# Kernel tuning notes

Hardware: AMD Instinct MI355X
Metric: run time of the kernel (lower is better)

Reference implementation:

```python
import jax, jax.numpy as jnp
import numpy as np

T, B, I, H = 2048, 128, 10, 512  # timesteps, batch, input_size, hidden_size


def setup_inputs() -> dict:
    key = jax.random.key(0)
    ks = jax.random.split(key, 7)
    s = 1.0 / np.sqrt(H)  # torch LSTMCell default init scale
    return {
        "x": jax.random.normal(ks[0], (T, B, I), dtype=jnp.float32),
        "hx": jax.random.normal(ks[1], (B, H), dtype=jnp.float32) * 0.1,
        "cx": jax.random.normal(ks[2], (B, H), dtype=jnp.float32) * 0.1,
        "W_ih": jax.random.uniform(ks[3], (4 * H, I), jnp.float32, -s, s),
        "W_hh": jax.random.uniform(ks[4], (4 * H, H), jnp.float32, -s, s),
        "b_ih": jax.random.uniform(ks[5], (4 * H,), jnp.float32, -s, s),
        "b_hh": jax.random.uniform(ks[6], (4 * H,), jnp.float32, -s, s),
    }


def reference(x, hx, cx, W_ih, W_hh, b_ih, b_hh):
    # Standard LSTMCell recurrence (PyTorch gate order: i, f, g, o).
    bias = b_ih + b_hh  # [4H]

    def step(carry, xt):
        h, c = carry  # [B,H], [B,H]
        gates = xt @ W_ih.T + h @ W_hh.T + bias  # [B,4H]
        i, f, g, o = jnp.split(gates, 4, axis=-1)
        i = jax.nn.sigmoid(i)
        f = jax.nn.sigmoid(f)
        g = jnp.tanh(g)
        o = jax.nn.sigmoid(o)
        c = f * c + i * g
        h = o * jnp.tanh(c)
        return (h, c), None

    (h, c), _ = jax.lax.scan(step, (hx, cx), x)  # scan over T
    # Original returns (x, (hx, cx)) where x == final hx.
    return (h, (h, c))
```

## Files before the change

### kernel.cpp

```cpp
#include <hip/hip_runtime.h>
#include <hip/hip_fp16.h>

#define T_STEPS 2048
#define B_SZ 128
#define I_SZ 10
#define H_SZ 512

#define NGRP 8
#define GWG 8
#define NWG (NGRP * GWG)
#define BSLICE 16
#define WCOL 64
#define NTHR 512

typedef _Float16 f16x8 __attribute__((ext_vector_type(8)));
typedef float f32x4 __attribute__((ext_vector_type(4)));
typedef float f32x2 __attribute__((ext_vector_type(2)));
typedef unsigned u32x4 __attribute__((ext_vector_type(4)));
typedef unsigned u32x2 __attribute__((ext_vector_type(2)));
typedef unsigned long long u64t;

__global__ void clear_hbuf_kernel(u64t* p) {
    const int i = blockIdx.x * 256 + threadIdx.x;
    #pragma unroll
    for (int k = 0; k < 4; ++k)
        __hip_atomic_store(p + i + k * 16384, 0ull,
                           __ATOMIC_RELAXED, __HIP_MEMORY_SCOPE_AGENT);
}

__global__ __launch_bounds__(NTHR, 2) void lstm_persistent(
    const float* __restrict__ x,
    const float* __restrict__ hx,
    const float* __restrict__ cx,
    const float* __restrict__ W_ih,
    const float* __restrict__ W_hh,
    const float* __restrict__ b_ih,
    const float* __restrict__ b_hh,
    float* __restrict__ out,
    u64t* hbuf)
{
    __shared__ _Float16 h_stage[BSLICE][520];
    __shared__ float lds_g[4 * WCOL][17];

    const int wg   = blockIdx.x;
    const int g    = wg >> 3;
    const int wgin = wg & 7;
    const int tid  = threadIdx.x;
    const int wid  = tid >> 6;
    const int lane = tid & 63;
    const int fr_col = lane & 15;
    const int fr_kg  = lane >> 4;

    int gcL[2], wr[2];
    #pragma unroll
    for (int f = 0; f < 2; ++f) {
        gcL[f] = wid * 32 + f * 16 + fr_col;
        wr[f]  = (gcL[f] >> 6) * H_SZ + wgin * WCOL + (gcL[f] & 63);
    }

    f16x8 wf[2][16];
    #pragma unroll
    for (int f = 0; f < 2; ++f)
        #pragma unroll
        for (int c = 0; c < 16; ++c) {
            const float* p = W_hh + (size_t)wr[f] * H_SZ + c * 32 + fr_kg * 8;
            f16x8 w;
            #pragma unroll
            for (int e = 0; e < 8; ++e) w[e] = (_Float16)p[e];
            wf[f][c] = w;
        }

    float wih[2][I_SZ], bias[2];
    #pragma unroll
    for (int f = 0; f < 2; ++f) {
        #pragma unroll
        for (int i = 0; i < I_SZ; ++i) wih[f][i] = W_ih[wr[f] * I_SZ + i];
        bias[f] = b_ih[wr[f]] + b_hh[wr[f]];
    }

    const int orow  = tid >> 5;
    const int ocol  = wgin * WCOL + 2 * (tid & 31);
    const int gbrow = g * BSLICE + orow;
    const size_t my_q = (size_t)orow * 256 + (ocol >> 1);

    float c0 = cx[gbrow * H_SZ + ocol];
    float c1 = cx[gbrow * H_SZ + ocol + 1];
    float h0 = hx[gbrow * H_SZ + ocol];
    float h1 = hx[gbrow * H_SZ + ocol + 1];

    int   st_row[4], st_p[4];
    bool  st_own[4];
    #pragma unroll
    for (int j = 0; j < 4; ++j) {
        const int q = wid * 512 + j * 128 + lane * 2;
        st_row[j] = q >> 8;
        st_p[j]   = q & 255;
        st_own[j] = ((st_p[j] >> 5) == wgin);
    }

    const int sent_idx = 15 * 256 + (lane & 7) * 32 + 31;

    {
        u64t* hb0 = hbuf + (size_t)g * (BSLICE * 256);
        union { _Float16 hp[2]; unsigned u; } pk;
        pk.hp[0] = (_Float16)h0; pk.hp[1] = (_Float16)h1;
        __hip_atomic_store(hb0 + my_q, ((u64t)1u << 32) | pk.u,
                           __ATOMIC_RELAXED, __HIP_MEMORY_SCOPE_AGENT);
        *(unsigned*)&h_stage[orow][ocol] = pk.u;
    }

    #pragma unroll 1
    for (int t = 0; t < T_STEPS; ++t) {
        f32x4 acc[2];
        #pragma unroll
        for (int r = 0; r < 4; ++r) {
            const int grow = g * BSLICE + fr_kg * 4 + r;
            const f32x2* xp = (const f32x2*)(x + ((size_t)t * B_SZ + grow) * I_SZ);
            const f32x2 a0 = xp[0], a1 = xp[1], a2 = xp[2], a3 = xp[3], a4 = xp[4];
            #pragma unroll
            for (int f = 0; f < 2; ++f) {
                float s = bias[f];
                s += a0.x*wih[f][0] + a0.y*wih[f][1] + a1.x*wih[f][2] + a1.y*wih[f][3]
                   + a2.x*wih[f][4] + a2.y*wih[f][5] + a3.x*wih[f][6] + a3.y*wih[f][7]
                   + a4.x*wih[f][8] + a4.y*wih[f][9];
                acc[f][r] = s;
            }
        }

        const u64t* hb = hbuf + ((size_t)(t & 1) * NGRP + g) * (BSLICE * 256);
        const unsigned tgt = (unsigned)(t + 1);

        if (wid == 0) {
            const u64t* sp = hb + sent_idx;
            for (;;) {
                u64t sv = __hip_atomic_load(sp, __ATOMIC_RELAXED,
                                            __HIP_MEMORY_SCOPE_AGENT);
                if (__all((unsigned)(sv >> 32) >= tgt)) break;
                __builtin_amdgcn_s_sleep(1);
            }
        }
        __syncthreads();

        {
            const char* sp = (const char*)hb + wid * 4096 + lane * 16;
            u32x4 q0, q1, q2, q3;
            bool done = false;
            for (;;) {
                if (!done) {
                    asm volatile(
                        "global_load_dwordx4 %0, %4, off sc0 sc1\n\t"
                        "global_load_dwordx4 %1, %4, off offset:1024 sc0 sc1\n\t"
                        "global_load_dwordx4 %2, %4, off offset:2048 sc0 sc1\n\t"
                        "global_load_dwordx4 %3, %4, off offset:3072 sc0 sc1\n\t"
                        "s_waitcnt vmcnt(0)"
                        : "=&v"(q0), "=&v"(q1), "=&v"(q2), "=&v"(q3)
                        : "v"(sp) : "memory");
                    done = (st_own[0] || (q0.y >= tgt && q0.w >= tgt)) &&
                           (st_own[1] || (q1.y >= tgt && q1.w >= tgt)) &&
                           (st_own[2] || (q2.y >= tgt && q2.w >= tgt)) &&
                           (st_own[3] || (q3.y >= tgt && q3.w >= tgt));
                }
                if (__all(done)) break;
                __builtin_amdgcn_s_sleep(1);
            }
            if (!st_own[0]) *(u32x2*)&h_stage[st_row[0]][st_p[0] * 2] = (u32x2){q0.x, q0.z};
            if (!st_own[1]) *(u32x2*)&h_stage[st_row[1]][st_p[1] * 2] = (u32x2){q1.x, q1.z};
            if (!st_own[2]) *(u32x2*)&h_stage[st_row[2]][st_p[2] * 2] = (u32x2){q2.x, q2.z};
            if (!st_own[3]) *(u32x2*)&h_stage[st_row[3]][st_p[3] * 2] = (u32x2){q3.x, q3.z};
        }
        __syncthreads();

        #pragma unroll
        for (int c = 0; c < 16; ++c) {
            const f16x8 a = *(const f16x8*)&h_stage[fr_col][c * 32 + fr_kg * 8];
            acc[0] = __builtin_amdgcn_mfma_f32_16x16x32_f16(a, wf[0][c], acc[0], 0, 0, 0);
            acc[1] = __builtin_amdgcn_mfma_f32_16x16x32_f16(a, wf[1][c], acc[1], 0, 0, 0);
        }

        #pragma unroll
        for (int f = 0; f < 2; ++f)
            #pragma unroll
            for (int r = 0; r < 4; ++r)
                lds_g[gcL[f]][fr_kg * 4 + r] = acc[f][r];
        __syncthreads();

        {
            const int cl = 2 * (tid & 31);
            const float i0 = lds_g[0 * WCOL + cl][orow],     f0 = lds_g[1 * WCOL + cl][orow];
            const float g0 = lds_g[2 * WCOL + cl][orow],     o0 = lds_g[3 * WCOL + cl][orow];
            const float i1 = lds_g[0 * WCOL + cl + 1][orow], f1 = lds_g[1 * WCOL + cl + 1][orow];
            const float g1 = lds_g[2 * WCOL + cl + 1][orow], o1 = lds_g[3 * WCOL + cl + 1][orow];

            const float ig0 = 1.f / (1.f + __expf(-i0));
            const float fg0 = 1.f / (1.f + __expf(-f0));
            const float eg0 = __expf(-2.f * g0);
            const float tg0 = (1.f - eg0) / (1.f + eg0);
            const float og0 = 1.f / (1.f + __expf(-o0));
            const float ig1 = 1.f / (1.f + __expf(-i1));
            const float fg1 = 1.f / (1.f + __expf(-f1));
            const float eg1 = __expf(-2.f * g1);
            const float tg1 = (1.f - eg1) / (1.f + eg1);
            const float og1 = 1.f / (1.f + __expf(-o1));

            c0 = fg0 * c0 + ig0 * tg0;
            c1 = fg1 * c1 + ig1 * tg1;
            const float e0 = __expf(-2.f * c0), e1 = __expf(-2.f * c1);
            h0 = og0 * (1.f - e0) / (1.f + e0);
            h1 = og1 * (1.f - e1) / (1.f + e1);

            if (t < T_STEPS - 1) {
                u64t* hbn = hbuf + ((size_t)((t + 1) & 1) * NGRP + g) * (BSLICE * 256);
                union { _Float16 hp[2]; unsigned u; } pk;
                pk.hp[0] = (_Float16)h0; pk.hp[1] = (_Float16)h1;
                __hip_atomic_store(hbn + my_q,
                                   ((u64t)(unsigned)(t + 2) << 32) | pk.u,
                                   __ATOMIC_RELAXED, __HIP_MEMORY_SCOPE_AGENT);
                *(unsigned*)&h_stage[orow][ocol] = pk.u;
            }
        }
    }

    out[gbrow * H_SZ + ocol]                       = h0;
    out[gbrow * H_SZ + ocol + 1]                   = h1;
    out[B_SZ * H_SZ + gbrow * H_SZ + ocol]         = h0;
    out[B_SZ * H_SZ + gbrow * H_SZ + ocol + 1]     = h1;
    out[2 * B_SZ * H_SZ + gbrow * H_SZ + ocol]     = c0;
    out[2 * B_SZ * H_SZ + gbrow * H_SZ + ocol + 1] = c1;
}

extern "C" void kernel_launch(void* const* d_in, const int* in_sizes, int n_in,
                              void* d_out, int out_size, void* d_ws, size_t ws_size,
                              hipStream_t stream) {
    const float* x    = (const float*)d_in[0];
    const float* hx   = (const float*)d_in[1];
    const float* cx   = (const float*)d_in[2];
    const float* W_ih = (const float*)d_in[3];
    const float* W_hh = (const float*)d_in[4];
    const float* b_ih = (const float*)d_in[5];
    const float* b_hh = (const float*)d_in[6];
    float* out = (float*)d_out;

    u64t* hbuf = (u64t*)d_ws;

    clear_hbuf_kernel<<<64, 256, 0, stream>>>(hbuf);
    lstm_persistent<<<NWG, NTHR, 0, stream>>>(x, hx, cx, W_ih, W_hh, b_ih, b_hh,
                                              out, hbuf);
}
```

Baseline: 6.492 ms.

## Compute all four gates per wave to remove LDS gate exchange and a barrier

Each wave now owns 16 hidden columns across all four gates (i,f,g,o), so its MFMA accumulators hold every gate needed for the cell update. The LDS gate-transpose buffer and one __syncthreads per timestep go away, and the block shrinks to 256 threads with 4x16 f16 weight fragments held in registers. Each wave also stages all of h from global memory, including its own columns, with eight loads per poll instead of four. The cost is higher register pressure per thread and a few lane shuffles to pack h pairs before the tagged stores.

Measured after the change: 7.337 ms. 13.0% more time.

```diff
diff --git a/kernel.cpp b/kernel.cpp
--- a/kernel.cpp
+++ b/kernel.cpp
@@ -11,7 +11,7 @@
 #define NWG (NGRP * GWG)
 #define BSLICE 16
 #define WCOL 64
-#define NTHR 512
+#define NTHR 256
 
 typedef _Float16 f16x8 __attribute__((ext_vector_type(8)));
 typedef float f32x4 __attribute__((ext_vector_type(4)));
@@ -28,7 +28,7 @@
                            __ATOMIC_RELAXED, __HIP_MEMORY_SCOPE_AGENT);
 }
 
-__global__ __launch_bounds__(NTHR, 2) void lstm_persistent(
+__global__ __launch_bounds__(NTHR, 1) void lstm_persistent(
     const float* __restrict__ x,
     const float* __restrict__ hx,
     const float* __restrict__ cx,
@@ -40,7 +40,6 @@
     u64t* hbuf)
 {
     __shared__ _Float16 h_stage[BSLICE][520];
-    __shared__ float lds_g[4 * WCOL][17];
 
     const int wg   = blockIdx.x;
     const int g    = wg >> 3;
@@ -51,79 +50,75 @@
     const int fr_col = lane & 15;
     const int fr_kg  = lane >> 4;
 
-    int gcL[2], wr[2];
-    #pragma unroll
-    for (int f = 0; f < 2; ++f) {
-        gcL[f] = wid * 32 + f * 16 + fr_col;
-        wr[f]  = (gcL[f] >> 6) * H_SZ + wgin * WCOL + (gcL[f] & 63);
-    }
-
-    f16x8 wf[2][16];
-    #pragma unroll
-    for (int f = 0; f < 2; ++f)
+    const int colL = wid * 16 + fr_col;
+    const int gcol = wgin * WCOL + colL;
+
+    f16x8 wf[4][16];
+    #pragma unroll
+    for (int gt = 0; gt < 4; ++gt)
         #pragma unroll
         for (int c = 0; c < 16; ++c) {
-            const float* p = W_hh + (size_t)wr[f] * H_SZ + c * 32 + fr_kg * 8;
+            const float* p = W_hh + (size_t)(gt * H_SZ + gcol) * H_SZ + c * 32 + fr_kg * 8;
             f16x8 w;
             #pragma unroll
             for (int e = 0; e < 8; ++e) w[e] = (_Float16)p[e];
-            wf[f][c] = w;
-        }
-
-    float wih[2][I_SZ], bias[2];
-    #pragma unroll
-    for (int f = 0; f < 2; ++f) {
-        #pragma unroll
-        for (int i = 0; i < I_SZ; ++i) wih[f][i] = W_ih[wr[f] * I_SZ + i];
-        bias[f] = b_ih[wr[f]] + b_hh[wr[f]];
-    }
-
-    const int orow  = tid >> 5;
-    const int ocol  = wgin * WCOL + 2 * (tid & 31);
-    const int gbrow = g * BSLICE + orow;
-    const size_t my_q = (size_t)orow * 256 + (ocol >> 1);
-
-    float c0 = cx[gbrow * H_SZ + ocol];
-    float c1 = cx[gbrow * H_SZ + ocol + 1];
-    float h0 = hx[gbrow * H_SZ + ocol];
-    float h1 = hx[gbrow * H_SZ + ocol + 1];
-
-    int   st_row[4], st_p[4];
-    bool  st_own[4];
-    #pragma unroll
-    for (int j = 0; j < 4; ++j) {
-        const int q = wid * 512 + j * 128 + lane * 2;
-        st_row[j] = q >> 8;
-        st_p[j]   = q & 255;
-        st_own[j] = ((st_p[j] >> 5) == wgin);
-    }
+            wf[gt][c] = w;
+        }
+
+    float wih[4][I_SZ], bias[4];
+    #pragma unroll
+    for (int gt = 0; gt < 4; ++gt) {
+        #pragma unroll
+        for (int i = 0; i < I_SZ; ++i) wih[gt][i] = W_ih[(gt * H_SZ + gcol) * I_SZ + i];
+        bias[gt] = b_ih[gt * H_SZ + gcol] + b_hh[gt * H_SZ + gcol];
+    }
+
+    float cst[4], hst[4];
+    #pragma unroll
+    for (int r = 0; r < 4; ++r) {
+        const int gbrow = g * BSLICE + fr_kg * 4 + r;
+        cst[r] = cx[gbrow * H_SZ + gcol];
+        hst[r] = hx[gbrow * H_SZ + gcol];
+    }
+
+    const int cp = wgin * 32 + wid * 8 + (fr_col >> 1);
+    const bool odd = (fr_col & 1);
+    const int prow0 = fr_kg * 4 + (odd ? 2 : 0);
 
     const int sent_idx = 15 * 256 + (lane & 7) * 32 + 31;
 
     {
         u64t* hb0 = hbuf + (size_t)g * (BSLICE * 256);
-        union { _Float16 hp[2]; unsigned u; } pk;
-        pk.hp[0] = (_Float16)h0; pk.hp[1] = (_Float16)h1;
-        __hip_atomic_store(hb0 + my_q, ((u64t)1u << 32) | pk.u,
-                           __ATOMIC_RELAXED, __HIP_MEMORY_SCOPE_AGENT);
-        *(unsigned*)&h_stage[orow][ocol] = pk.u;
+        #pragma unroll
+        for (int j = 0; j < 2; ++j) {
+            const float give = odd ? hst[j] : hst[2 + j];
+            const float hp   = __shfl_xor(give, 1);
+            const float own  = odd ? hst[2 + j] : hst[j];
+            const float lo = odd ? hp : own;
+            const float hi = odd ? own : hp;
+            union { _Float16 f[2]; unsigned u; } pk;
+            pk.f[0] = (_Float16)lo; pk.f[1] = (_Float16)hi;
+            __hip_atomic_store(hb0 + (size_t)(prow0 + j) * 256 + cp,
+                               ((u64t)1u << 32) | pk.u,
+                               __ATOMIC_RELAXED, __HIP_MEMORY_SCOPE_AGENT);
+        }
     }
 
     #pragma unroll 1
     for (int t = 0; t < T_STEPS; ++t) {
-        f32x4 acc[2];
+        f32x4 acc[4];
         #pragma unroll
         for (int r = 0; r < 4; ++r) {
             const int grow = g * BSLICE + fr_kg * 4 + r;
             const f32x2* xp = (const f32x2*)(x + ((size_t)t * B_SZ + grow) * I_SZ);
             const f32x2 a0 = xp[0], a1 = xp[1], a2 = xp[2], a3 = xp[3], a4 = xp[4];
             #pragma unroll
-            for (int f = 0; f < 2; ++f) {
-                float s = bias[f];
-                s += a0.x*wih[f][0] + a0.y*wih[f][1] + a1.x*wih[f][2] + a1.y*wih[f][3]
-                   + a2.x*wih[f][4] + a2.y*wih[f][5] + a3.x*wih[f][6] + a3.y*wih[f][7]
-                   + a4.x*wih[f][8] + a4.y*wih[f][9];
-                acc[f][r] = s;
+            for (int gt = 0; gt < 4; ++gt) {
+                float s = bias[gt];
+                s += a0.x*wih[gt][0] + a0.y*wih[gt][1] + a1.x*wih[gt][2] + a1.y*wih[gt][3]
+                   + a2.x*wih[gt][4] + a2.y*wih[gt][5] + a3.x*wih[gt][6] + a3.y*wih[gt][7]
+                   + a4.x*wih[gt][8] + a4.y*wih[gt][9];
+                acc[gt][r] = s;
             }
         }
 
@@ -142,90 +137,96 @@
         __syncthreads();
 
         {
-            const char* sp = (const char*)hb + wid * 4096 + lane * 16;
-            u32x4 q0, q1, q2, q3;
+            const char* spA = (const char*)hb + wid * 8192 + lane * 16;
+            const char* spB = spA + 4096;
+            u32x4 q0, q1, q2, q3, q4, q5, q6, q7;
             bool done = false;
             for (;;) {
                 if (!done) {
                     asm volatile(
-                        "global_load_dwordx4 %0, %4, off sc0 sc1\n\t"
-                        "global_load_dwordx4 %1, %4, off offset:1024 sc0 sc1\n\t"
-                        "global_load_dwordx4 %2, %4, off offset:2048 sc0 sc1\n\t"
-                        "global_load_dwordx4 %3, %4, off offset:3072 sc0 sc1\n\t"
+                        "global_load_dwordx4 %0, %8, off sc0 sc1\n\t"
+                        "global_load_dwordx4 %1, %8, off offset:1024 sc0 sc1\n\t"
+                        "global_load_dwordx4 %2, %8, off offset:2048 sc0 sc1\n\t"
+                        "global_load_dwordx4 %3, %8, off offset:3072 sc0 sc1\n\t"
+                        "global_load_dwordx4 %4, %9, off sc0 sc1\n\t"
+                        "global_load_dwordx4 %5, %9, off offset:1024 sc0 sc1\n\t"
+                        "global_load_dwordx4 %6, %9, off offset:2048 sc0 sc1\n\t"
+                        "global_load_dwordx4 %7, %9, off offset:3072 sc0 sc1\n\t"
                         "s_waitcnt vmcnt(0)"
-                        : "=&v"(q0), "=&v"(q1), "=&v"(q2), "=&v"(q3)
-                        : "v"(sp) : "memory");
-                    done = (st_own[0] || (q0.y >= tgt && q0.w >= tgt)) &&
-                           (st_own[1] || (q1.y >= tgt && q1.w >= tgt)) &&
-                           (st_own[2] || (q2.y >= tgt && q2.w >= tgt)) &&
-                           (st_own[3] || (q3.y >= tgt && q3.w >= tgt));
+                        : "=&v"(q0), "=&v"(q1), "=&v"(q2), "=&v"(q3),
+                          "=&v"(q4), "=&v"(q5), "=&v"(q6), "=&v"(q7)
+                        : "v"(spA), "v"(spB) : "memory");
+                    done = (q0.y >= tgt && q0.w >= tgt) && (q1.y >= tgt && q1.w >= tgt) &&
+                           (q2.y >= tgt && q2.w >= tgt) && (q3.y >= tgt && q3.w >= tgt) &&
+                           (q4.y >= tgt && q4.w >= tgt) && (q5.y >= tgt && q5.w >= tgt) &&
+                           (q6.y >= tgt && q6.w >= tgt) && (q7.y >= tgt && q7.w >= tgt);
                 }
                 if (__all(done)) break;
                 __builtin_amdgcn_s_sleep(1);
             }
-            if (!st_own[0]) *(u32x2*)&h_stage[st_row[0]][st_p[0] * 2] = (u32x2){q0.x, q0.z};
-            if (!st_own[1]) *(u32x2*)&h_stage[st_row[1]][st_p[1] * 2] = (u32x2){q1.x, q1.z};
-            if (!st_own[2]) *(u32x2*)&h_stage[st_row[2]][st_p[2] * 2] = (u32x2){q2.x, q2.z};
-            if (!st_own[3]) *(u32x2*)&h_stage[st_row[3]][st_p[3] * 2] = (u32x2){q3.x, q3.z};
+            const int qb = wid * 1024 + lane * 2;
+            #pragma unroll
+            for (int m = 0; m < 8; ++m) {
+                const int q = qb + m * 128;
+                const int row = q >> 8, p = q & 255;
+                u32x4 qq;
+                switch (m) {
+                    case 0: qq = q0; break; case 1: qq = q1; break;
+                    case 2: qq = q2; break; case 3: qq = q3; break;
+                    case 4: qq = q4; break; case 5: qq = q5; break;
+                    case 6: qq = q6; break; default: qq = q7; break;
+                }
+                *(u32x2*)&h_stage[row][p * 2] = (u32x2){qq.x, qq.z};
+            }
         }
         __syncthreads();
 
         #pragma unroll
         for (int c = 0; c < 16; ++c) {
             const f16x8 a = *(const f16x8*)&h_stage[fr_col][c * 32 + fr_kg * 8];
-            acc[0] = __builtin_amdgcn_mfma_f32_16x16x32_f16(a, wf[0][c], acc[0], 0, 0, 0);
-            acc[1] = __builtin_amdgcn_mfma_f32_16x16x32_f16(a, wf[1][c], acc[1], 0, 0, 0);
-        }
-
-        #pragma unroll
-        for (int f = 0; f < 2; ++f)
-            #pragma unroll
-            for (int r = 0; r < 4; ++r)
-                lds_g[gcL[f]][fr_kg * 4 + r] = acc[f][r];
-        __syncthreads();
-
-        {
-            const int cl = 2 * (tid & 31);
-            const float i0 = lds_g[0 * WCOL + cl][orow],     f0 = lds_g[1 * WCOL + cl][orow];
-            const float g0 = lds_g[2 * WCOL + cl][orow],     o0 = lds_g[3 * WCOL + cl][orow];
-            const float i1 = lds_g[0 * WCOL + cl + 1][orow], f1 = lds_g[1 * WCOL + cl + 1][orow];
-            const float g1 = lds_g[2 * WCOL + cl + 1][orow], o1 = lds_g[3 * WCOL + cl + 1][orow];
-
-            const float ig0 = 1.f / (1.f + __expf(-i0));
-            const float fg0 = 1.f / (1.f + __expf(-f0));
-            const float eg0 = __expf(-2.f * g0);
-            const float tg0 = (1.f - eg0) / (1.f + eg0);
-            const float og0 = 1.f / (1.f + __expf(-o0));
-            const float ig1 = 1.f / (1.f + __expf(-i1));
-            const float fg1 = 1.f / (1.f + __expf(-f1));
-            const float eg1 = __expf(-2.f * g1);
-            const float tg1 = (1.f - eg1) / (1.f + eg1);
-            const float og1 = 1.f / (1.f + __expf(-o1));
-
-            c0 = fg0 * c0 + ig0 * tg0;
-            c1 = fg1 * c1 + ig1 * tg1;
-            const float e0 = __expf(-2.f * c0), e1 = __expf(-2.f * c1);
-            h0 = og0 * (1.f - e0) / (1.f + e0);
-            h1 = og1 * (1.f - e1) / (1.f + e1);
-
-            if (t < T_STEPS - 1) {
-                u64t* hbn = hbuf + ((size_t)((t + 1) & 1) * NGRP + g) * (BSLICE * 256);
-                union { _Float16 hp[2]; unsigned u; } pk;
-                pk.hp[0] = (_Float16)h0; pk.hp[1] = (_Float16)h1;
-                __hip_atomic_store(hbn + my_q,
-                                   ((u64t)(unsigned)(t + 2) << 32) | pk.u,
+            #pragma unroll
+            for (int gt = 0; gt < 4; ++gt)
+                acc[gt] = __builtin_amdgcn_mfma_f32_16x16x32_f16(a, wf[gt][c], acc[gt], 0, 0, 0);
+        }
+
+        #pragma unroll
+        for (int r = 0; r < 4; ++r) {
+            const float ig = 1.f / (1.f + __expf(-acc[0][r]));
+            const float fg = 1.f / (1.f + __expf(-acc[1][r]));
+            const float eg = __expf(-2.f * acc[2][r]);
+            const float tg = (1.f - eg) / (1.f + eg);
+            const float og = 1.f / (1.f + __expf(-acc[3][r]));
+            cst[r] = fg * cst[r] + ig * tg;
+            const float ec = __expf(-2.f * cst[r]);
+            hst[r] = og * (1.f - ec) / (1.f + ec);
+        }
+
+        if (t < T_STEPS - 1) {
+            u64t* hbn = hbuf + ((size_t)((t + 1) & 1) * NGRP + g) * (BSLICE * 256);
+            const u64t tagw = (u64t)(unsigned)(t + 2) << 32;
+            #pragma unroll
+            for (int j = 0; j < 2; ++j) {
+                const float give = odd ? hst[j] : hst[2 + j];
+                const float hp   = __shfl_xor(give, 1);
+                const float own  = odd ? hst[2 + j] : hst[j];
+                const float lo = odd ? hp : own;
+                const float hi = odd ? own : hp;
+                union { _Float16 f[2]; unsigned u; } pk;
+                pk.f[0] = (_Float16)lo; pk.f[1] = (_Float16)hi;
+                __hip_atomic_store(hbn + (size_t)(prow0 + j) * 256 + cp,
+                                   tagw | pk.u,
                                    __ATOMIC_RELAXED, __HIP_MEMORY_SCOPE_AGENT);
-                *(unsigned*)&h_stage[orow][ocol] = pk.u;
-            }
-        }
-    }
-
-    out[gbrow * H_SZ + ocol]                       = h0;
-    out[gbrow * H_SZ + ocol + 1]                   = h1;
-    out[B_SZ * H_SZ + gbrow * H_SZ + ocol]         = h0;
-    out[B_SZ * H_SZ + gbrow * H_SZ + ocol + 1]     = h1;
-    out[2 * B_SZ * H_SZ + gbrow * H_SZ + ocol]     = c0;
-    out[2 * B_SZ * H_SZ + gbrow * H_SZ + ocol + 1] = c1;
+            }
+        }
+    }
+
+    #pragma unroll
+    for (int r = 0; r < 4; ++r) {
+        const int gbrow = g * BSLICE + fr_kg * 4 + r;
+        out[gbrow * H_SZ + gcol]                   = hst[r];
+        out[B_SZ * H_SZ + gbrow * H_SZ + gcol]     = hst[r];
+        out[2 * B_SZ * H_SZ + gbrow * H_SZ + gcol] = cst[r];
+    }
 }
 
 extern "C" void kernel_launch(void* const* d_in, const int* in_sizes, int n_in,
```

## Split h exchange into two halves and overlap second-half loads with MFMAs

Applied to the files above, without the earlier changes.

The per-step hidden-state gather is split into two K halves. All four loads are issued up front, but the kernel only waits for the first half, runs the first 8 MFMA chunks, then waits for and validates the second half before the remaining MFMAs. This is meant to hide global-load latency and the cross-workgroup polling behind compute. The cost is an extra __syncthreads per step, plus a remapped staging layout and ownership tests that must exactly match the producer's layout.

Result: no change. 6.539 ms (+0.7%).

```diff
diff --git a/kernel.cpp b/kernel.cpp
--- a/kernel.cpp
+++ b/kernel.cpp
@@ -88,15 +88,8 @@
     float h0 = hx[gbrow * H_SZ + ocol];
     float h1 = hx[gbrow * H_SZ + ocol + 1];
 
-    int   st_row[4], st_p[4];
-    bool  st_own[4];
-    #pragma unroll
-    for (int j = 0; j < 4; ++j) {
-        const int q = wid * 512 + j * 128 + lane * 2;
-        st_row[j] = q >> 8;
-        st_p[j]   = q & 255;
-        st_own[j] = ((st_p[j] >> 5) == wgin);
-    }
+    const bool own0 = ((lane >> 4) == wgin);
+    const bool own1 = ((lane >> 4) + 4 == wgin);
 
     const int sent_idx = 15 * 256 + (lane & 7) * 32 + 31;
 
@@ -141,37 +134,75 @@
         }
         __syncthreads();
 
+        const char* sp = (const char*)hb + wid * 4096 + lane * 16;
+        u32x4 q0, q1, q2, q3;
+        asm volatile(
+            "global_load_dwordx4 %0, %4, off sc0 sc1\n\t"
+            "global_load_dwordx4 %1, %4, off offset:2048 sc0 sc1\n\t"
+            "global_load_dwordx4 %2, %4, off offset:1024 sc0 sc1\n\t"
+            "global_load_dwordx4 %3, %4, off offset:3072 sc0 sc1\n\t"
+            "s_waitcnt vmcnt(2)"
+            : "=&v"(q0), "=&v"(q1), "=&v"(q2), "=&v"(q3)
+            : "v"(sp) : "memory");
+        __builtin_amdgcn_sched_barrier(0);
+
         {
-            const char* sp = (const char*)hb + wid * 4096 + lane * 16;
-            u32x4 q0, q1, q2, q3;
-            bool done = false;
+            bool ok = own0 || (q0.y >= tgt && q0.w >= tgt &&
+                               q1.y >= tgt && q1.w >= tgt);
             for (;;) {
-                if (!done) {
+                if (__all(ok)) break;
+                __builtin_amdgcn_s_sleep(1);
+                if (!ok) {
                     asm volatile(
-                        "global_load_dwordx4 %0, %4, off sc0 sc1\n\t"
-                        "global_load_dwordx4 %1, %4, off offset:1024 sc0 sc1\n\t"
-                        "global_load_dwordx4 %2, %4, off offset:2048 sc0 sc1\n\t"
-                        "global_load_dwordx4 %3, %4, off offset:3072 sc0 sc1\n\t"
+                        "global_load_dwordx4 %0, %2, off sc0 sc1\n\t"
+                        "global_load_dwordx4 %1, %2, off offset:2048 sc0 sc1\n\t"
                         "s_waitcnt vmcnt(0)"
-                        : "=&v"(q0), "=&v"(q1), "=&v"(q2), "=&v"(q3)
-                        : "v"(sp) : "memory");
-                    done = (st_own[0] || (q0.y >= tgt && q0.w >= tgt)) &&
-                           (st_own[1] || (q1.y >= tgt && q1.w >= tgt)) &&
-                           (st_own[2] || (q2.y >= tgt && q2.w >= tgt)) &&
-                           (st_own[3] || (q3.y >= tgt && q3.w >= tgt));
+                        : "+v"(q0), "+v"(q1) : "v"(sp) : "memory");
+                    ok = (q0.y >= tgt && q0.w >= tgt &&
+                          q1.y >= tgt && q1.w >= tgt);
                 }
-                if (__all(done)) break;
+            }
+            if (!own0) {
+                *(u32x2*)&h_stage[2 * wid][lane * 4]     = (u32x2){q0.x, q0.z};
+                *(u32x2*)&h_stage[2 * wid + 1][lane * 4] = (u32x2){q1.x, q1.z};
+            }
+        }
+        __syncthreads();
+
+        #pragma unroll
+        for (int c = 0; c < 8; ++c) {
+            const f16x8 a = *(const f16x8*)&h_stage[fr_col][c * 32 + fr_kg * 8];
+            acc[0] = __builtin_amdgcn_mfma_f32_16x16x32_f16(a, wf[0][c], acc[0], 0, 0, 0);
+            acc[1] = __builtin_amdgcn_mfma_f32_16x16x32_f16(a, wf[1][c], acc[1], 0, 0, 0);
+        }
+
+        asm volatile("s_waitcnt vmcnt(0)" : "+v"(q2), "+v"(q3) :: "memory");
+        __builtin_amdgcn_sched_barrier(0);
+        {
+            bool ok = own1 || (q2.y >= tgt && q2.w >= tgt &&
+                               q3.y >= tgt && q3.w >= tgt);
+            for (;;) {
+                if (__all(ok)) break;
                 __builtin_amdgcn_s_sleep(1);
-            }
-            if (!st_own[0]) *(u32x2*)&h_stage[st_row[0]][st_p[0] * 2] = (u32x2){q0.x, q0.z};
-            if (!st_own[1]) *(u32x2*)&h_stage[st_row[1]][st_p[1] * 2] = (u32x2){q1.x, q1.z};
-            if (!st_own[2]) *(u32x2*)&h_stage[st_row[2]][st_p[2] * 2] = (u32x2){q2.x, q2.z};
-            if (!st_own[3]) *(u32x2*)&h_stage[st_row[3]][st_p[3] * 2] = (u32x2){q3.x, q3.z};
-        }
-        __syncthreads();
-
-        #pragma unroll
-        for (int c = 0; c < 16; ++c) {
+                if (!ok) {
+                    asm volatile(
+                        "global_load_dwordx4 %0, %2, off offset:1024 sc0 sc1\n\t"
+                        "global_load_dwordx4 %1, %2, off offset:3072 sc0 sc1\n\t"
+                        "s_waitcnt vmcnt(0)"
+                        : "+v"(q2), "+v"(q3) : "v"(sp) : "memory");
+                    ok = (q2.y >= tgt && q2.w >= tgt &&
+                          q3.y >= tgt && q3.w >= tgt);
+                }
+            }
+            if (!own1) {
+                *(u32x2*)&h_stage[2 * wid][256 + lane * 4]     = (u32x2){q2.x, q2.z};
+                *(u32x2*)&h_stage[2 * wid + 1][256 + lane * 4] = (u32x2){q3.x, q3.z};
+            }
+        }
+        __syncthreads();
+
+        #pragma unroll
+        for (int c = 8; c < 16; ++c) {
             const f16x8 a = *(const f16x8*)&h_stage[fr_col][c * 32 + fr_kg * 8];
             acc[0] = __builtin_amdgcn_mfma_f32_16x16x32_f16(a, wf[0][c], acc[0], 0, 0, 0);
             acc[1] = __builtin_amdgcn_mfma_f32_16x16x32_f16(a, wf[1][c], acc[1], 0, 0, 0);
```
